# Kernel tuning notes

Hardware: AMD Instinct MI355X
Metric: run time of the kernel (lower is better)

Reference implementation:

```python
import jax, jax.numpy as jnp
import numpy as np

COS_EPS = 1e-8      # torch F.cosine_similarity default eps
NORM_EPS = 1e-16    # renormalization eps in address()


def setup_inputs() -> dict:
    B, N, M = 64, 16384, 64
    key = jax.random.key(0)
    ks = jax.random.split(key, 7)
    key_vector = jax.random.normal(ks[0], (B, M), dtype=jnp.float32)
    key_strength = jax.random.uniform(ks[1], (B, 1), dtype=jnp.float32) * 5.0
    gate = jax.random.uniform(ks[2], (B, 1), dtype=jnp.float32)
    shift_raw = jax.random.uniform(ks[3], (B, 3), dtype=jnp.float32)
    shift = shift_raw / jnp.sum(shift_raw, axis=1, keepdims=True)  # softmax-like shift dist
    sharpen = 1.0 + jax.random.uniform(ks[4], (B, 1), dtype=jnp.float32)  # >= 1 as in NTM
    la_raw = jax.random.uniform(ks[5], (B, N), dtype=jnp.float32)
    last_address = la_raw / jnp.sum(la_raw, axis=1, keepdims=True)  # valid weighting
    memory = jax.random.normal(ks[6], (B, N, M), dtype=jnp.float32) * 0.1
    return {
        "key_vector": key_vector,
        "key_strength": key_strength,
        "gate": gate,
        "shift": shift,
        "sharpen": sharpen,
        "last_address": last_address,
        "memory": memory,
    }


def reference(key_vector, key_strength, gate, shift, sharpen, last_address, memory):
    # --- content addressing: cosine similarity of key vs every memory row ---
    dot = jnp.einsum("bm,bnm->bn", key_vector, memory)            # [B, N]
    k_norm = jnp.linalg.norm(key_vector, axis=-1, keepdims=True)  # [B, 1]
    m_norm = jnp.linalg.norm(memory, axis=-1)                     # [B, N]
    cos = dot / jnp.maximum(k_norm * m_norm, COS_EPS)
    wc = jax.nn.softmax(key_strength * cos, axis=1)               # [B, N]
    # --- interpolation gate ---
    wg = gate * wc + (1.0 - gate) * last_address                  # [B, N]
    # --- circular convolution with size-3 shift kernel ---
    # torch conv1d is cross-correlation: ws[j] = s0*w[j-1] + s1*w[j] + s2*w[j+1] (circular)
    ws = (shift[:, 0:1] * jnp.roll(wg, 1, axis=1)
          + shift[:, 1:2] * wg
          + shift[:, 2:3] * jnp.roll(wg, -1, axis=1))             # [B, N]
    # --- sharpening + renormalization ---
    ws = ws ** sharpen
    wt = ws / (jnp.sum(ws, axis=1, keepdims=True) + NORM_EPS)
    return wt
```

## Files before the change

### kernel.cpp

```cpp
#include <hip/hip_runtime.h>
#include <math.h>

#define B_ 64
#define N_ 16384
#define M_ 64

typedef float vfloat4 __attribute__((ext_vector_type(4)));

__global__ __launch_bounds__(256) void scores_kernel(
    const float* __restrict__ key, const float* __restrict__ beta,
    const float* __restrict__ memory, float* __restrict__ s_out)
{
    const int b    = blockIdx.y;
    const int tid  = threadIdx.x;
    const int lane = tid & 63;
    const int wave = tid >> 6;
    const int l    = lane & 3;
    const int rr   = lane >> 2;

    vfloat4 k4[4];
#pragma unroll
    for (int j = 0; j < 4; ++j)
        k4[j] = *reinterpret_cast<const vfloat4*>(key + b * M_ + j * 16 + l * 4);

    float ksq = 0.f;
#pragma unroll
    for (int j = 0; j < 4; ++j)
        ksq += k4[j].x * k4[j].x + k4[j].y * k4[j].y + k4[j].z * k4[j].z + k4[j].w * k4[j].w;
    ksq += __shfl_xor(ksq, 1);
    ksq += __shfl_xor(ksq, 2);
    const float knorm = sqrtf(ksq);
    const float kb    = beta[b];

    const float* __restrict__ mb = memory + (size_t)b * N_ * M_;
    float* __restrict__ sb       = s_out + (size_t)b * N_;

    const int rowBase = blockIdx.x * 256 + wave * 64;
#pragma unroll
    for (int t = 0; t < 4; ++t) {
        const int row = rowBase + t * 16 + rr;
        const float* rp = mb + (size_t)row * M_;
        vfloat4 m4[4];
#pragma unroll
        for (int j = 0; j < 4; ++j)
            m4[j] = __builtin_nontemporal_load(
                reinterpret_cast<const vfloat4*>(rp + j * 16 + l * 4));

        float dot = 0.f, msq = 0.f;
#pragma unroll
        for (int j = 0; j < 4; ++j) {
            dot += k4[j].x * m4[j].x + k4[j].y * m4[j].y + k4[j].z * m4[j].z + k4[j].w * m4[j].w;
            msq += m4[j].x * m4[j].x + m4[j].y * m4[j].y + m4[j].z * m4[j].z + m4[j].w * m4[j].w;
        }
        dot += __shfl_xor(dot, 1);  dot += __shfl_xor(dot, 2);
        msq += __shfl_xor(msq, 1);  msq += __shfl_xor(msq, 2);

        if (l == 0) {
            const float denom = fmaxf(knorm * sqrtf(msq), 1e-8f);
            sb[row] = expf(kb * dot / denom);
        }
    }
}

__global__ __launch_bounds__(1024) void addr_kernel(
    const float* __restrict__ gate, const float* __restrict__ shift,
    const float* __restrict__ sharpen, const float* __restrict__ la,
    float* __restrict__ out)
{
    const int b    = blockIdx.x;
    const int t    = threadIdx.x;
    const int lane = t & 63;
    const int wv   = t >> 6;

    __shared__ float red[16];
    __shared__ float lft[1024];
    __shared__ float rgt[1024];

    float* __restrict__ ob        = out + (size_t)b * N_;
    const float* __restrict__ lab = la + (size_t)b * N_;

    float s[16];
#pragma unroll
    for (int q = 0; q < 4; ++q)
        *reinterpret_cast<float4*>(&s[4 * q]) =
            reinterpret_cast<const float4*>(ob)[t * 4 + q];

    float zs = 0.f;
#pragma unroll
    for (int i = 0; i < 16; ++i) zs += s[i];
#pragma unroll
    for (int m = 1; m < 64; m <<= 1) zs += __shfl_xor(zs, m);
    if (lane == 0) red[wv] = zs;
    __syncthreads();
    float Z = red[0];
#pragma unroll
    for (int i = 1; i < 16; ++i) Z += red[i];
    __syncthreads();
    const float invZ = 1.0f / Z;

    const float gg = gate[b];
    const float om = 1.0f - gg;
    float wl[16];
#pragma unroll
    for (int q = 0; q < 4; ++q)
        *reinterpret_cast<float4*>(&wl[4 * q]) =
            reinterpret_cast<const float4*>(lab)[t * 4 + q];
    float wg[16];
#pragma unroll
    for (int i = 0; i < 16; ++i) wg[i] = gg * (s[i] * invZ) + om * wl[i];

    lft[t] = wg[0];
    rgt[t] = wg[15];
    __syncthreads();
    const float prev = rgt[(t + 1023) & 1023];
    const float nxt  = lft[(t + 1) & 1023];
    const float s0 = shift[b * 3 + 0];
    const float s1 = shift[b * 3 + 1];
    const float s2 = shift[b * 3 + 2];
    float ws[16];
    ws[0] = s0 * prev + s1 * wg[0] + s2 * wg[1];
#pragma unroll
    for (int i = 1; i < 15; ++i) ws[i] = s0 * wg[i - 1] + s1 * wg[i] + s2 * wg[i + 1];
    ws[15] = s0 * wg[14] + s1 * wg[15] + s2 * nxt;

    const float p = sharpen[b];
    float ssum = 0.f;
#pragma unroll
    for (int i = 0; i < 16; ++i) { ws[i] = exp2f(p * log2f(ws[i])); ssum += ws[i]; }
#pragma unroll
    for (int m = 1; m < 64; m <<= 1) ssum += __shfl_xor(ssum, m);
    __syncthreads();
    if (lane == 0) red[wv] = ssum;
    __syncthreads();
    float S = red[0];
#pragma unroll
    for (int i = 1; i < 16; ++i) S += red[i];
    const float inv = 1.0f / (S + 1e-16f);

#pragma unroll
    for (int q = 0; q < 4; ++q) {
        float4 o;
        o.x = ws[4 * q + 0] * inv;
        o.y = ws[4 * q + 1] * inv;
        o.z = ws[4 * q + 2] * inv;
        o.w = ws[4 * q + 3] * inv;
        reinterpret_cast<float4*>(ob)[t * 4 + q] = o;
    }
}

extern "C" void kernel_launch(void* const* d_in, const int* in_sizes, int n_in,
                              void* d_out, int out_size, void* d_ws, size_t ws_size,
                              hipStream_t stream) {
    const float* key     = (const float*)d_in[0];
    const float* beta    = (const float*)d_in[1];
    const float* gate    = (const float*)d_in[2];
    const float* shift   = (const float*)d_in[3];
    const float* sharpen = (const float*)d_in[4];
    const float* la      = (const float*)d_in[5];
    const float* memory  = (const float*)d_in[6];
    float* out = (float*)d_out;

    dim3 gridA(N_ / 256, B_);
    scores_kernel<<<gridA, 256, 0, stream>>>(key, beta, memory, out);

    addr_kernel<<<B_, 1024, 0, stream>>>(gate, shift, sharpen, la, out);
}
```

Baseline: 357.4 us.

## Fuse scoring and addressing into one cooperative kernel with grid-wide syncs

```diff
diff --git a/kernel.cpp b/kernel.cpp
--- a/kernel.cpp
+++ b/kernel.cpp
@@ -1,28 +1,45 @@
 #include <hip/hip_runtime.h>
+#include <hip/hip_cooperative_groups.h>
 #include <math.h>
 
 #define B_ 64
 #define N_ 16384
 #define M_ 64
 
+namespace cg = cooperative_groups;
+
 typedef float vfloat4 __attribute__((ext_vector_type(4)));
 
-__global__ __launch_bounds__(256) void scores_kernel(
+__global__ __launch_bounds__(1024, 4) void ntm_fused(
     const float* __restrict__ key, const float* __restrict__ beta,
-    const float* __restrict__ memory, float* __restrict__ s_out)
+    const float* __restrict__ gate, const float* __restrict__ shift,
+    const float* __restrict__ sharpen, const float* __restrict__ la,
+    const float* __restrict__ memory, float* __restrict__ out,
+    float* __restrict__ wsp)
 {
-    const int b    = blockIdx.y;
-    const int tid  = threadIdx.x;
-    const int lane = tid & 63;
-    const int wave = tid >> 6;
+    const int blk  = blockIdx.x;
+    const int b    = blk >> 2;
+    const int q    = blk & 3;
+    const int R0   = q << 12;
+    const int t    = threadIdx.x;
+    const int lane = t & 63;
+    const int w    = t >> 6;
     const int l    = lane & 3;
     const int rr   = lane >> 2;
+
+    __shared__ float sc[4096];
+    __shared__ float wred[16];
+    __shared__ float bx[8];
+    __shared__ float lft[1024], rgt[1024];
+
+    float* zpart = wsp;
+    float* spart = wsp + 256;
+    float* bsc   = wsp + 512;
 
     vfloat4 k4[4];
 #pragma unroll
     for (int j = 0; j < 4; ++j)
         k4[j] = *reinterpret_cast<const vfloat4*>(key + b * M_ + j * 16 + l * 4);
-
     float ksq = 0.f;
 #pragma unroll
     for (int j = 0; j < 4; ++j)
@@ -32,120 +49,109 @@
     const float knorm = sqrtf(ksq);
     const float kb    = beta[b];
 
-    const float* __restrict__ mb = memory + (size_t)b * N_ * M_;
-    float* __restrict__ sb       = s_out + (size_t)b * N_;
+    const float* __restrict__ mb = memory + ((size_t)b * N_ + R0) * M_;
 
-    const int rowBase = blockIdx.x * 256 + wave * 64;
-#pragma unroll
-    for (int t = 0; t < 4; ++t) {
-        const int row = rowBase + t * 16 + rr;
-        const float* rp = mb + (size_t)row * M_;
+    float zs = 0.f;
+    const int waveBase = w << 8;
+#pragma unroll 4
+    for (int it = 0; it < 16; ++it) {
+        const int lr = waveBase + (it << 4) + rr;
+        const float* rp = mb + (size_t)lr * M_;
         vfloat4 m4[4];
 #pragma unroll
         for (int j = 0; j < 4; ++j)
             m4[j] = __builtin_nontemporal_load(
                 reinterpret_cast<const vfloat4*>(rp + j * 16 + l * 4));
-
         float dot = 0.f, msq = 0.f;
 #pragma unroll
         for (int j = 0; j < 4; ++j) {
             dot += k4[j].x * m4[j].x + k4[j].y * m4[j].y + k4[j].z * m4[j].z + k4[j].w * m4[j].w;
             msq += m4[j].x * m4[j].x + m4[j].y * m4[j].y + m4[j].z * m4[j].z + m4[j].w * m4[j].w;
         }
-        dot += __shfl_xor(dot, 1);  dot += __shfl_xor(dot, 2);
-        msq += __shfl_xor(msq, 1);  msq += __shfl_xor(msq, 2);
-
-        if (l == 0) {
-            const float denom = fmaxf(knorm * sqrtf(msq), 1e-8f);
-            sb[row] = expf(kb * dot / denom);
-        }
+        dot += __shfl_xor(dot, 1); dot += __shfl_xor(dot, 2);
+        msq += __shfl_xor(msq, 1); msq += __shfl_xor(msq, 2);
+        const float e = expf(kb * dot / fmaxf(knorm * sqrtf(msq), 1e-8f));
+        if (l == 0) sc[lr] = e;
+        zs += e;
     }
-}
-
-__global__ __launch_bounds__(1024) void addr_kernel(
-    const float* __restrict__ gate, const float* __restrict__ shift,
-    const float* __restrict__ sharpen, const float* __restrict__ la,
-    float* __restrict__ out)
-{
-    const int b    = blockIdx.x;
-    const int t    = threadIdx.x;
-    const int lane = t & 63;
-    const int wv   = t >> 6;
-
-    __shared__ float red[16];
-    __shared__ float lft[1024];
-    __shared__ float rgt[1024];
-
-    float* __restrict__ ob        = out + (size_t)b * N_;
-    const float* __restrict__ lab = la + (size_t)b * N_;
-
-    float s[16];
-#pragma unroll
-    for (int q = 0; q < 4; ++q)
-        *reinterpret_cast<float4*>(&s[4 * q]) =
-            reinterpret_cast<const float4*>(ob)[t * 4 + q];
-
-    float zs = 0.f;
-#pragma unroll
-    for (int i = 0; i < 16; ++i) zs += s[i];
 #pragma unroll
     for (int m = 1; m < 64; m <<= 1) zs += __shfl_xor(zs, m);
-    if (lane == 0) red[wv] = zs;
+    if (lane == 0) wred[w] = zs * 0.25f;
     __syncthreads();
-    float Z = red[0];
+    if (t == 0) {
+        float pz = 0.f;
 #pragma unroll
-    for (int i = 1; i < 16; ++i) Z += red[i];
+        for (int i = 0; i < 16; ++i) pz += wred[i];
+        __hip_atomic_store(&zpart[blk], pz, __ATOMIC_RELEASE, __HIP_MEMORY_SCOPE_AGENT);
+        __hip_atomic_store(&bsc[blk * 2 + 0], sc[0],    __ATOMIC_RELEASE, __HIP_MEMORY_SCOPE_AGENT);
+        __hip_atomic_store(&bsc[blk * 2 + 1], sc[4095], __ATOMIC_RELEASE, __HIP_MEMORY_SCOPE_AGENT);
+    }
+    cg::this_grid().sync();
+
+    if (t < 4)
+        bx[t] = __hip_atomic_load(&zpart[b * 4 + t], __ATOMIC_ACQUIRE, __HIP_MEMORY_SCOPE_AGENT);
+    if (t == 4) {
+        const int pblk = b * 4 + ((q + 3) & 3);
+        bx[4] = __hip_atomic_load(&bsc[pblk * 2 + 1], __ATOMIC_ACQUIRE, __HIP_MEMORY_SCOPE_AGENT);
+    }
+    if (t == 5) {
+        const int nblk = b * 4 + ((q + 1) & 3);
+        bx[5] = __hip_atomic_load(&bsc[nblk * 2 + 0], __ATOMIC_ACQUIRE, __HIP_MEMORY_SCOPE_AGENT);
+    }
     __syncthreads();
-    const float invZ = 1.0f / Z;
+    const float invZ = 1.0f / (bx[0] + bx[1] + bx[2] + bx[3]);
+    const float gg = gate[b], om = 1.0f - gg;
+    const float s0 = shift[b * 3 + 0], s1 = shift[b * 3 + 1], s2 = shift[b * 3 + 2];
 
-    const float gg = gate[b];
-    const float om = 1.0f - gg;
-    float wl[16];
-#pragma unroll
-    for (int q = 0; q < 4; ++q)
-        *reinterpret_cast<float4*>(&wl[4 * q]) =
-            reinterpret_cast<const float4*>(lab)[t * 4 + q];
-    float wg[16];
-#pragma unroll
-    for (int i = 0; i < 16; ++i) wg[i] = gg * (s[i] * invZ) + om * wl[i];
+    const float4 sv = *reinterpret_cast<const float4*>(sc + t * 4);
+    const float4 lv = *reinterpret_cast<const float4*>(la + (size_t)b * N_ + R0 + t * 4);
+    const float wg0 = gg * (sv.x * invZ) + om * lv.x;
+    const float wg1 = gg * (sv.y * invZ) + om * lv.y;
+    const float wg2 = gg * (sv.z * invZ) + om * lv.z;
+    const float wg3 = gg * (sv.w * invZ) + om * lv.w;
 
-    lft[t] = wg[0];
-    rgt[t] = wg[15];
+    lft[t] = wg0; rgt[t] = wg3;
     __syncthreads();
-    const float prev = rgt[(t + 1023) & 1023];
-    const float nxt  = lft[(t + 1) & 1023];
-    const float s0 = shift[b * 3 + 0];
-    const float s1 = shift[b * 3 + 1];
-    const float s2 = shift[b * 3 + 2];
-    float ws[16];
-    ws[0] = s0 * prev + s1 * wg[0] + s2 * wg[1];
-#pragma unroll
-    for (int i = 1; i < 15; ++i) ws[i] = s0 * wg[i - 1] + s1 * wg[i] + s2 * wg[i + 1];
-    ws[15] = s0 * wg[14] + s1 * wg[15] + s2 * nxt;
+    float prev, nxt;
+    if (t == 0) {
+        const int pr = (R0 - 1) & (N_ - 1);
+        prev = gg * (bx[4] * invZ) + om * la[(size_t)b * N_ + pr];
+    } else prev = rgt[t - 1];
+    if (t == 1023) {
+        const int nr = (R0 + 4096) & (N_ - 1);
+        nxt = gg * (bx[5] * invZ) + om * la[(size_t)b * N_ + nr];
+    } else nxt = lft[t + 1];
+
+    float w0 = s0 * prev + s1 * wg0 + s2 * wg1;
+    float w1 = s0 * wg0  + s1 * wg1 + s2 * wg2;
+    float w2 = s0 * wg1  + s1 * wg2 + s2 * wg3;
+    float w3 = s0 * wg2  + s1 * wg3 + s2 * nxt;
 
     const float p = sharpen[b];
-    float ssum = 0.f;
+    w0 = exp2f(p * log2f(w0));
+    w1 = exp2f(p * log2f(w1));
+    w2 = exp2f(p * log2f(w2));
+    w3 = exp2f(p * log2f(w3));
+    float ss = w0 + w1 + w2 + w3;
 #pragma unroll
-    for (int i = 0; i < 16; ++i) { ws[i] = exp2f(p * log2f(ws[i])); ssum += ws[i]; }
+    for (int m = 1; m < 64; m <<= 1) ss += __shfl_xor(ss, m);
+    if (lane == 0) wred[w] = ss;
+    __syncthreads();
+    if (t == 0) {
+        float ps = 0.f;
 #pragma unroll
-    for (int m = 1; m < 64; m <<= 1) ssum += __shfl_xor(ssum, m);
+        for (int i = 0; i < 16; ++i) ps += wred[i];
+        __hip_atomic_store(&spart[blk], ps, __ATOMIC_RELEASE, __HIP_MEMORY_SCOPE_AGENT);
+    }
+    cg::this_grid().sync();
+
+    if (t < 4)
+        bx[t] = __hip_atomic_load(&spart[b * 4 + t], __ATOMIC_ACQUIRE, __HIP_MEMORY_SCOPE_AGENT);
     __syncthreads();
-    if (lane == 0) red[wv] = ssum;
-    __syncthreads();
-    float S = red[0];
-#pragma unroll
-    for (int i = 1; i < 16; ++i) S += red[i];
-    const float inv = 1.0f / (S + 1e-16f);
-
-#pragma unroll
-    for (int q = 0; q < 4; ++q) {
-        float4 o;
-        o.x = ws[4 * q + 0] * inv;
-        o.y = ws[4 * q + 1] * inv;
-        o.z = ws[4 * q + 2] * inv;
-        o.w = ws[4 * q + 3] * inv;
-        reinterpret_cast<float4*>(ob)[t * 4 + q] = o;
-    }
+    const float inv = 1.0f / (bx[0] + bx[1] + bx[2] + bx[3] + 1e-16f);
+    float4 o;
+    o.x = w0 * inv; o.y = w1 * inv; o.z = w2 * inv; o.w = w3 * inv;
+    *reinterpret_cast<float4*>(out + (size_t)b * N_ + R0 + t * 4) = o;
 }
 
 extern "C" void kernel_launch(void* const* d_in, const int* in_sizes, int n_in,
@@ -159,9 +165,11 @@
     const float* la      = (const float*)d_in[5];
     const float* memory  = (const float*)d_in[6];
     float* out = (float*)d_out;
+    float* wsf = (float*)d_ws;
 
-    dim3 gridA(N_ / 256, B_);
-    scores_kernel<<<gridA, 256, 0, stream>>>(key, beta, memory, out);
-
-    addr_kernel<<<B_, 1024, 0, stream>>>(gate, shift, sharpen, la, out);
+    void* args[] = { (void*)&key, (void*)&beta, (void*)&gate, (void*)&shift,
+                     (void*)&sharpen, (void*)&la, (void*)&memory,
+                     (void*)&out, (void*)&wsf };
+    hipLaunchCooperativeKernel((const void*)ntm_fused, dim3(256), dim3(1024),
+                               args, 0, stream);
 }
```

Result: slower. 457.2 us (+27.9%).
